# Kernel tuning notes

Hardware: AMD Instinct MI355X
Metric: run time of the kernel (lower is better)

The kernel has to match this reference:

```python
import jax, jax.numpy as jnp
import numpy as np

BN_EPS = 1e-5


def _pool_features(labels, fx, fy, n_labels):
    # Mean-pool per-pixel features (fx, fy, xx, yy coord maps) over superpixel labels.
    B, _, w, h = labels.shape
    xx = (jnp.arange(w, dtype=jnp.float32) / (w - 1)) * 2.0 - 1.0   # varies along dim 2
    yy = (jnp.arange(h, dtype=jnp.float32) / (h - 1)) * 2.0 - 1.0   # varies along dim 3
    xx_map = jnp.broadcast_to(xx[:, None], (w, h))
    yy_map = jnp.broadcast_to(yy[None, :], (w, h))
    P = w * h
    feats = jnp.stack([
        fx[:, 0].reshape(B, P),
        fy[:, 0].reshape(B, P),
        jnp.broadcast_to(xx_map.reshape(1, P), (B, P)),
        jnp.broadcast_to(yy_map.reshape(1, P), (B, P)),
    ], axis=-1).reshape(B * P, 4)                                   # [B*P, 4]
    seg = (labels[:, 0].reshape(B, P)
           + n_labels * jnp.arange(B, dtype=jnp.int32)[:, None]).reshape(-1)
    sums = jax.ops.segment_sum(feats, seg, num_segments=B * n_labels)        # [B*K, 4]
    counts = jax.ops.segment_sum(jnp.ones((B * P,), jnp.float32), seg,
                                 num_segments=B * n_labels)                  # [B*K]
    return sums / jnp.maximum(counts, 1.0)[:, None]


def _bn(x, g, b):
    # BatchNorm1d in training mode: batch statistics over the token dim.
    m = x.mean(axis=0)
    v = x.var(axis=0)
    return (x - m) * jax.lax.rsqrt(v + BN_EPS) * g + b


def reference(labels, fx, fy, frame_idx, n_frames, n_labels,
              conv_w, conv_b, bn1_g, bn1_b, lin_w, lin_b, bn2_g, bn2_b):
    pooled = _pool_features(labels, fx, fy, n_labels)               # [B*K, 4] = (fx, fy, xx, yy)
    t = jnp.repeat(frame_idx.astype(jnp.float32) / (n_frames - 1), n_labels)  # [B*K]
    x = jnp.concatenate([t[:, None], pooled], axis=1)               # [B*K, 5]
    x = x @ conv_w.T + conv_b                                       # Conv1d(5,64,1) == linear
    x = jax.nn.relu(_bn(x, bn1_g, bn1_b))
    x = x @ lin_w.T + lin_b                                         # Linear(64,32)
    x = jax.nn.relu(_bn(x, bn2_g, bn2_b))
    nrm = jnp.linalg.norm(x, axis=1, keepdims=True)
    return x / jnp.maximum(nrm, 1e-8)


def setup_inputs() -> dict:
    key = jax.random.key(0)
    ks = jax.random.split(key, 12)
    B, H, W, K = 16, 512, 512, 1024
    labels = jax.random.randint(ks[0], (B, 1, H, W), 0, K, dtype=jnp.int32)
    fx = jax.random.normal(ks[1], (B, 1, H, W), dtype=jnp.float32)
    fy = jax.random.normal(ks[2], (B, 1, H, W), dtype=jnp.float32)
    frame_idx = jax.random.randint(ks[3], (B,), 0, 100, dtype=jnp.int32)
    conv_w = jax.random.normal(ks[4], (64, 5), dtype=jnp.float32) * 0.3
    conv_b = jax.random.normal(ks[5], (64,), dtype=jnp.float32) * 0.05
    bn1_g = 1.0 + 0.05 * jax.random.normal(ks[6], (64,), dtype=jnp.float32)
    bn1_b = 0.05 * jax.random.normal(ks[7], (64,), dtype=jnp.float32)
    lin_w = jax.random.normal(ks[8], (32, 64), dtype=jnp.float32) * 0.1
    lin_b = jax.random.normal(ks[9], (32,), dtype=jnp.float32) * 0.05
    bn2_g = 1.0 + 0.05 * jax.random.normal(ks[10], (32,), dtype=jnp.float32)
    bn2_b = 0.05 * jax.random.normal(ks[11], (32,), dtype=jnp.float32)
    return {"labels": labels, "fx": fx, "fy": fy, "frame_idx": frame_idx,
            "n_frames": 100, "n_labels": K,
            "conv_w": conv_w, "conv_b": conv_b, "bn1_g": bn1_g, "bn1_b": bn1_b,
            "lin_w": lin_w, "lin_b": lin_b, "bn2_g": bn2_g, "bn2_b": bn2_b}
```

## Files before the change

kernel.cpp:

```cpp
#include <hip/hip_runtime.h>
#include <math.h>

#define TPB 256
#define TPBP 1024
#define FSCALE 16384.0f
#define INV_FSCALE (1.0f / 16384.0f)
#define FBIAS (1 << 17)
#define FCLAMP 7.0f


__global__ __launch_bounds__(TPBP)
void pool_kernel(const int* __restrict__ labels,
                 const float* __restrict__ fx,
                 const float* __restrict__ fy,
                 float* __restrict__ partial,
                 int K, int H, int W, int wlog, int chunks) {
    extern __shared__ unsigned long long sh[];
    unsigned long long* geo = sh;
    unsigned long long* fxy = sh + K;
    const int tid = threadIdx.x;

    for (int i = tid; i < K; i += TPBP) { geo[i] = 0ull; fxy[i] = 0ull; }
    __syncthreads();

    const int P = H * W;
    const int b = blockIdx.x / chunks;
    const int chunk = blockIdx.x - b * chunks;
    const int chunkP = P / chunks;
    const size_t base = (size_t)b * P + (size_t)chunk * chunkP;
    const int4*   l4p  = (const int4*)(labels + base);
    const float4* fx4p = (const float4*)(fx + base);
    const float4* fy4p = (const float4*)(fy + base);
    const int nvec = chunkP >> 2;

    for (int v = tid; v < nvec; v += TPBP) {
        int4   l4 = l4p[v];
        float4 f4 = fx4p[v];
        float4 g4 = fy4p[v];
        int p0 = chunk * chunkP + (v << 2);
        int   ls[4] = {l4.x, l4.y, l4.z, l4.w};
        float fs[4] = {f4.x, f4.y, f4.z, f4.w};
        float gs[4] = {g4.x, g4.y, g4.z, g4.w};
        #pragma unroll
        for (int s = 0; s < 4; ++s) {
            int p = p0 + s;
            int i, j;
            if (wlog >= 0) { i = p >> wlog; j = p & (W - 1); }
            else           { i = p / W;     j = p - i * W; }
            unsigned long long gadd = ((unsigned long long)i << 40)
                                    | ((unsigned long long)j << 16) | 1ull;
            int qx = __float2int_rn(fminf(fmaxf(fs[s], -FCLAMP), FCLAMP) * FSCALE) + FBIAS;
            int qy = __float2int_rn(fminf(fmaxf(gs[s], -FCLAMP), FCLAMP) * FSCALE) + FBIAS;
            unsigned long long fadd = ((unsigned long long)(unsigned int)qx << 32)
                                    | (unsigned long long)(unsigned int)qy;
            atomicAdd(&geo[ls[s]], gadd);
            atomicAdd(&fxy[ls[s]], fadd);
        }
    }
    __syncthreads();

    const float sx = 2.f / (float)(H - 1);
    const float sy = 2.f / (float)(W - 1);
    float* outp = partial + (size_t)blockIdx.x * K * 5;
    for (int k = tid; k < K; k += TPBP) {
        unsigned long long g = geo[k];
        unsigned long long ff = fxy[k];
        unsigned int ci = (unsigned int)(g & 0xFFFFull);
        float cnt = (float)ci;
        float sj  = (float)(unsigned int)((g >> 16) & 0xFFFFFFull);
        float si  = (float)(unsigned int)(g >> 40);
        long long cbias = (long long)ci << 17;
        outp[0 * K + k] = (float)((long long)(ff >> 32) - cbias) * INV_FSCALE;
        outp[1 * K + k] = (float)((long long)(ff & 0xFFFFFFFFull) - cbias) * INV_FSCALE;
        outp[2 * K + k] = sx * si - cnt;
        outp[3 * K + k] = sy * sj - cnt;
        outp[4 * K + k] = cnt;
    }
}

template <int ROWS>
__device__ __forceinline__ float red_fixed(const float* __restrict__ base, int stride) {
    float a = 0.f;
    #pragma unroll
    for (int r = 0; r < ROWS; ++r) a += base[(size_t)r * stride];
    return a;
}
__device__ __forceinline__ float red_dyn(const float* __restrict__ base, int rows, int stride) {
    float a = 0.f;
    #pragma unroll 8
    for (int r = 0; r < rows; ++r) a += base[(size_t)r * stride];
    return a;
}

__global__ __launch_bounds__(TPB)
void k_layer1(const float* __restrict__ partial,
              const int* __restrict__ frame_idx,
              const int* __restrict__ n_frames_p,
              const float* __restrict__ conv_w,
              const float* __restrict__ conv_b,
              float* __restrict__ statA,
              float* __restrict__ h1g,
              int K, int N, int chunks) {
    __shared__ float red[320];
    __shared__ float cw[320], cb[64];
    __shared__ float h1t[64 * 65];
    __shared__ float ps[256], pq[256];

    const int tid = threadIdx.x;
    const int bid = blockIdx.x;

    for (int i = tid; i < 320; i += TPB) cw[i] = conv_w[i];
    if (tid < 64) cb[tid] = conv_b[tid];

    const int t0 = bid * 64;
    const int b  = t0 / K;
    const int k0 = t0 - b * K;

    const int f1 = tid >> 6, kk = tid & 63;
    float a0 = 0.f, a1 = 0.f;
    const float* pb = partial + (size_t)b * chunks * K * 5;
    if (chunks == 16) {
        #pragma unroll
        for (int ch = 0; ch < 16; ++ch) {
            const float* pc = pb + (size_t)ch * K * 5;
            a0 += pc[(size_t)f1 * K + k0 + kk];
            if (tid < 64) a1 += pc[(size_t)4 * K + k0 + tid];
        }
    } else {
        #pragma unroll 4
        for (int ch = 0; ch < chunks; ++ch) {
            const float* pc = pb + (size_t)ch * K * 5;
            a0 += pc[(size_t)f1 * K + k0 + kk];
            if (tid < 64) a1 += pc[(size_t)4 * K + k0 + tid];
        }
    }
    red[f1 * 64 + kk] = a0;
    if (tid < 64) red[4 * 64 + tid] = a1;
    __syncthreads();

    const int g  = tid >> 6;
    const int tt = tid & 63;
    const int t  = t0 + tt;
    const bool valid = t < N;

    const float cntv = red[4 * 64 + tt];
    const float inv  = 1.f / fmaxf(cntv, 1.f);
    const float invnf = 1.f / (float)(n_frames_p[0] - 1);
    const float x0 = valid ? (float)frame_idx[b] * invnf : 0.f;
    const float x1 = red[0 * 64 + tt] * inv;
    const float x2 = red[1 * 64 + tt] * inv;
    const float x3 = red[2 * 64 + tt] * inv;
    const float x4 = red[3 * 64 + tt] * inv;

    const int c0 = g * 16;
    #pragma unroll
    for (int j = 0; j < 16; ++j) {
        int c = c0 + j;
        const float* w = cw + c * 5;
        float h = cb[c] + w[0]*x0 + w[1]*x1 + w[2]*x2 + w[3]*x3 + w[4]*x4;
        h1g[(size_t)c * N + t] = h;
        h1t[c * 65 + tt] = valid ? h : 0.f;
    }
    __syncthreads();

    {
        const int cc = tid & 63, rr = tid >> 6;
        float s = 0.f, q = 0.f;
        #pragma unroll
        for (int i = 0; i < 16; ++i) {
            float v = h1t[cc * 65 + rr * 16 + i];
            s += v; q += v * v;
        }
        ps[rr * 64 + cc] = s;
        pq[rr * 64 + cc] = q;
    }
    __syncthreads();
    if (tid < 64) {
        float su = ps[tid] + ps[64 + tid] + ps[128 + tid] + ps[192 + tid];
        float sq = pq[tid] + pq[64 + tid] + pq[128 + tid] + pq[192 + tid];
        statA[(size_t)bid * 128 + tid] = su;
        statA[(size_t)bid * 128 + 64 + tid] = sq;
    }
}

__global__ __launch_bounds__(TPB)
void k_layer2(const float* __restrict__ statA,
              const float* __restrict__ bn1_g,
              const float* __restrict__ bn1_b,
              const float* __restrict__ lin_w,
              const float* __restrict__ lin_b,
              const float* __restrict__ h1g,
              float* __restrict__ statB,
              float* __restrict__ h2g,
              int N) {
    __shared__ float red[256], w2[2048], lb[32];
    __shared__ float sc1[64], sh1[64];
    __shared__ float h1t[64 * 64];
    __shared__ float h2t[32 * 65];
    __shared__ float ps[256], pq[256];

    const int tid = threadIdx.x;
    const int bid = blockIdx.x;
    const int nblk = gridDim.x;
    const int t0 = bid * 64;

    for (int i = tid; i < 2048; i += TPB) w2[i] = lin_w[i];
    if (tid < 32) lb[tid] = lin_b[tid];

    {
        const int col  = tid & 127;
        const int half = tid >> 7;
        const int rows = nblk >> 1;
        const float* base = statA + (size_t)half * rows * 128 + col;
        red[tid] = (rows == 128) ? red_fixed<128>(base, 128)
                                 : red_dyn(base, rows, 128);
    }

    {
        #pragma unroll
        for (int pass = 0; pass < 4; ++pass) {
            int idx = pass * TPB + tid;
            int c = idx >> 4, q = idx & 15;
            float4 v = *(const float4*)(h1g + (size_t)c * N + t0 + q * 4);
            *(float4*)(&h1t[c * 64 + q * 4]) = v;
        }
    }
    __syncthreads();

    if (tid < 64) {
        float su = red[tid] + red[128 + tid];
        float sq = red[64 + tid] + red[192 + tid];
        float invN = 1.f / (float)N;
        float mean = su * invN;
        float var  = sq * invN - mean * mean;
        float s = bn1_g[tid] * rsqrtf(var + 1e-5f);
        sc1[tid] = s;
        sh1[tid] = bn1_b[tid] - mean * s;
    }
    __syncthreads();

    const int g  = tid >> 6;
    const int tt = tid & 63;
    const int t  = t0 + tt;
    const bool valid = t < N;

    float y[64];
    #pragma unroll
    for (int c = 0; c < 64; ++c)
        y[c] = fmaxf(h1t[c * 64 + tt] * sc1[c] + sh1[c], 0.f);

    const int o0 = g * 8;
    #pragma unroll
    for (int j = 0; j < 8; ++j) {
        int o = o0 + j;
        const float* wo = w2 + o * 64;
        float acc = lb[o];
        #pragma unroll
        for (int c = 0; c < 64; ++c) acc += wo[c] * y[c];
        h2g[(size_t)o * N + t] = acc;
        h2t[o * 65 + tt] = valid ? acc : 0.f;
    }
    __syncthreads();

    {
        const int o = tid & 31, rr = tid >> 5;
        float s = 0.f, q = 0.f;
        #pragma unroll
        for (int i = 0; i < 8; ++i) {
            float v = h2t[o * 65 + rr * 8 + i];
            s += v; q += v * v;
        }
        ps[rr * 32 + o] = s;
        pq[rr * 32 + o] = q;
    }
    __syncthreads();
    if (tid < 32) {
        float su = 0.f, sq = 0.f;
        #pragma unroll
        for (int rr = 0; rr < 8; ++rr) { su += ps[rr * 32 + tid]; sq += pq[rr * 32 + tid]; }
        statB[(size_t)bid * 64 + tid] = su;
        statB[(size_t)bid * 64 + 32 + tid] = sq;
    }
}

__global__ __launch_bounds__(TPB)
void k_final(const float* __restrict__ statB,
             const float* __restrict__ bn2_g,
             const float* __restrict__ bn2_b,
             const float* __restrict__ h2g,
             float* __restrict__ out,
             int N) {
    __shared__ float red[256];
    __shared__ float sc2[32], sh2[32];
    __shared__ float h2t[32 * 68];
    __shared__ float ssqp[4 * 64], linv[64];

    const int tid = threadIdx.x;
    const int bid = blockIdx.x;
    const int nblk = gridDim.x;
    const int t0 = bid * 64;

    {
        const int col = tid & 63;
        const int qr  = tid >> 6;
        const int rows = nblk >> 2;
        const float* base = statB + (size_t)qr * rows * 64 + col;
        red[tid] = (rows == 64) ? red_fixed<64>(base, 64)
                                : red_dyn(base, rows, 64);
    }

    {
        #pragma unroll
        for (int pass = 0; pass < 2; ++pass) {
            int idx = pass * TPB + tid;
            int o = idx >> 4, q = idx & 15;
            float4 v = *(const float4*)(h2g + (size_t)o * N + t0 + q * 4);
            *(float4*)(&h2t[o * 68 + q * 4]) = v;
        }
    }
    __syncthreads();

    if (tid < 32) {
        float su = red[tid] + red[64 + tid] + red[128 + tid] + red[192 + tid];
        float sq = red[32 + tid] + red[96 + tid] + red[160 + tid] + red[224 + tid];
        float invN = 1.f / (float)N;
        float mean = su * invN;
        float var  = sq * invN - mean * mean;
        float s = bn2_g[tid] * rsqrtf(var + 1e-5f);
        sc2[tid] = s;
        sh2[tid] = bn2_b[tid] - mean * s;
    }
    __syncthreads();

    const int g  = tid >> 6;
    const int tt = tid & 63;
    {
        const int o0 = g * 8;
        float ss = 0.f;
        #pragma unroll
        for (int j = 0; j < 8; ++j) {
            int o = o0 + j;
            float v = fmaxf(h2t[o * 68 + tt] * sc2[o] + sh2[o], 0.f);
            h2t[o * 68 + tt] = v;
            ss += v * v;
        }
        ssqp[g * 64 + tt] = ss;
    }
    __syncthreads();
    if (g == 0) {
        float tot = ssqp[tt] + ssqp[64 + tt] + ssqp[128 + tt] + ssqp[192 + tt];
        linv[tt] = 1.f / fmaxf(sqrtf(tot), 1e-8f);
    }
    __syncthreads();

    const int nq = min(512, (N - t0) * 8);
    float4* o4 = (float4*)(out + (size_t)t0 * 32);
    for (int q = tid; q < nq; q += TPB) {
        int tk = q >> 3;
        int oo = (q & 7) * 4;
        float iv = linv[tk];
        o4[q] = make_float4(h2t[(oo + 0) * 68 + tk] * iv,
                            h2t[(oo + 1) * 68 + tk] * iv,
                            h2t[(oo + 2) * 68 + tk] * iv,
                            h2t[(oo + 3) * 68 + tk] * iv);
    }
}

extern "C" void kernel_launch(void* const* d_in, const int* in_sizes, int n_in,
                              void* d_out, int out_size, void* d_ws, size_t ws_size,
                              hipStream_t stream) {
    const int*   labels     = (const int*)d_in[0];
    const float* fx         = (const float*)d_in[1];
    const float* fy         = (const float*)d_in[2];
    const int*   frame_idx  = (const int*)d_in[3];
    const int*   n_frames_p = (const int*)d_in[4];
    const float* conv_w = (const float*)d_in[6];
    const float* conv_b = (const float*)d_in[7];
    const float* bn1_g  = (const float*)d_in[8];
    const float* bn1_b  = (const float*)d_in[9];
    const float* lin_w  = (const float*)d_in[10];
    const float* lin_b  = (const float*)d_in[11];
    const float* bn2_g  = (const float*)d_in[12];
    const float* bn2_b  = (const float*)d_in[13];
    float* out = (float*)d_out;

    const int B = in_sizes[3];
    const int P = in_sizes[0] / B;
    const int W = (int)(sqrt((double)P) + 0.5);
    const int H = P / W;
    const int K = out_size / (B * 32);
    const int N = B * K;

    int wlog = -1;
    if ((W & (W - 1)) == 0) { wlog = 0; while ((1 << wlog) < W) ++wlog; }

    const int nblk = (N + 63) / 64;

    int chunks = 16;
    while (chunks > 1 && (P % (chunks * 4)) != 0) chunks >>= 1;
    while (P / chunks > 16384) chunks <<= 1;

    float* statA   = (float*)d_ws;
    float* statB   = statA + (size_t)nblk * 128;
    float* partial = statB + (size_t)nblk * 64;
    float* h1g     = partial + (size_t)B * chunks * K * 5;
    float* h2g     = h1g + (size_t)64 * N;

    pool_kernel<<<B * chunks, TPBP, (size_t)K * 16, stream>>>(
        labels, fx, fy, partial, K, H, W, wlog, chunks);
    k_layer1<<<nblk, TPB, 0, stream>>>(
        partial, frame_idx, n_frames_p, conv_w, conv_b, statA, h1g, K, N, chunks);
    k_layer2<<<nblk, TPB, 0, stream>>>(
        statA, bn1_g, bn1_b, lin_w, lin_b, h1g, statB, h2g, N);
    k_final<<<nblk, TPB, 0, stream>>>(
        statB, bn2_g, bn2_b, h2g, out, N);
}
```

Baseline: 127.9 us.

## Derive BN1 statistics from input feature moments instead of materializing conv output

Layer 1 no longer writes the 64-channel conv output to global memory. It stores only the 5 pooled features per token, plus per-block first and second moments of those features (5 sums and 15 cross products). Layer 2 rebuilds the BN1 mean and variance algebraically from these moments and the conv weights, then recomputes the conv inline. This cuts global traffic from 64 floats per token to 5 and shrinks the statistics reduction, at the cost of recomputing the conv and some cancellation risk when variance is formed from raw second moments.

```diff
diff --git a/kernel.cpp b/kernel.cpp
--- a/kernel.cpp
+++ b/kernel.cpp
@@ -92,25 +92,22 @@
     return a;
 }
 
+__constant__ int PA[15] = {0,0,0,0,0, 1,1,1,1, 2,2,2, 3,3, 4};
+__constant__ int PB[15] = {0,1,2,3,4, 1,2,3,4, 2,3,4, 3,4, 4};
+
 __global__ __launch_bounds__(TPB)
-void k_layer1(const float* __restrict__ partial,
-              const int* __restrict__ frame_idx,
-              const int* __restrict__ n_frames_p,
-              const float* __restrict__ conv_w,
-              const float* __restrict__ conv_b,
-              float* __restrict__ statA,
-              float* __restrict__ h1g,
-              int K, int N, int chunks) {
+void k_feat(const float* __restrict__ partial,
+            const int* __restrict__ frame_idx,
+            const int* __restrict__ n_frames_p,
+            float* __restrict__ statM,
+            float* __restrict__ featg,
+            int K, int N, int chunks) {
     __shared__ float red[320];
-    __shared__ float cw[320], cb[64];
-    __shared__ float h1t[64 * 65];
-    __shared__ float ps[256], pq[256];
+    __shared__ float xls[5 * 65];
+    __shared__ float pm[8 * 32];
 
     const int tid = threadIdx.x;
     const int bid = blockIdx.x;
-
-    for (int i = tid; i < 320; i += TPB) cw[i] = conv_w[i];
-    if (tid < 64) cb[tid] = conv_b[tid];
 
     const int t0 = bid * 64;
     const int b  = t0 / K;
@@ -143,59 +140,70 @@
     const int t  = t0 + tt;
     const bool valid = t < N;
 
-    const float cntv = red[4 * 64 + tt];
-    const float inv  = 1.f / fmaxf(cntv, 1.f);
-    const float invnf = 1.f / (float)(n_frames_p[0] - 1);
-    const float x0 = valid ? (float)frame_idx[b] * invnf : 0.f;
-    const float x1 = red[0 * 64 + tt] * inv;
-    const float x2 = red[1 * 64 + tt] * inv;
-    const float x3 = red[2 * 64 + tt] * inv;
-    const float x4 = red[3 * 64 + tt] * inv;
-
-    const int c0 = g * 16;
-    #pragma unroll
-    for (int j = 0; j < 16; ++j) {
-        int c = c0 + j;
-        const float* w = cw + c * 5;
-        float h = cb[c] + w[0]*x0 + w[1]*x1 + w[2]*x2 + w[3]*x3 + w[4]*x4;
-        h1g[(size_t)c * N + t] = h;
-        h1t[c * 65 + tt] = valid ? h : 0.f;
-    }
-    __syncthreads();
-
-    {
-        const int cc = tid & 63, rr = tid >> 6;
-        float s = 0.f, q = 0.f;
-        #pragma unroll
-        for (int i = 0; i < 16; ++i) {
-            float v = h1t[cc * 65 + rr * 16 + i];
-            s += v; q += v * v;
-        }
-        ps[rr * 64 + cc] = s;
-        pq[rr * 64 + cc] = q;
-    }
-    __syncthreads();
-    if (tid < 64) {
-        float su = ps[tid] + ps[64 + tid] + ps[128 + tid] + ps[192 + tid];
-        float sq = pq[tid] + pq[64 + tid] + pq[128 + tid] + pq[192 + tid];
-        statA[(size_t)bid * 128 + tid] = su;
-        statA[(size_t)bid * 128 + 64 + tid] = sq;
+    if (g == 0) {
+        const float cntv = red[4 * 64 + tt];
+        const float inv  = 1.f / fmaxf(cntv, 1.f);
+        const float invnf = 1.f / (float)(n_frames_p[0] - 1);
+        const float x0 = valid ? (float)frame_idx[b] * invnf : 0.f;
+        const float x1 = red[0 * 64 + tt] * inv;
+        const float x2 = red[1 * 64 + tt] * inv;
+        const float x3 = red[2 * 64 + tt] * inv;
+        const float x4 = red[3 * 64 + tt] * inv;
+        if (valid) {
+            featg[(size_t)0 * N + t] = x0;
+            featg[(size_t)1 * N + t] = x1;
+            featg[(size_t)2 * N + t] = x2;
+            featg[(size_t)3 * N + t] = x3;
+            featg[(size_t)4 * N + t] = x4;
+        }
+        xls[0 * 65 + tt] = valid ? x0 : 0.f;
+        xls[1 * 65 + tt] = valid ? x1 : 0.f;
+        xls[2 * 65 + tt] = valid ? x2 : 0.f;
+        xls[3 * 65 + tt] = valid ? x3 : 0.f;
+        xls[4 * 65 + tt] = valid ? x4 : 0.f;
+    }
+    __syncthreads();
+
+    {
+        const int q = tid & 31, rr = tid >> 5;
+        float s = 0.f;
+        if (q < 5) {
+            #pragma unroll
+            for (int i = 0; i < 8; ++i) s += xls[q * 65 + rr * 8 + i];
+        } else if (q < 20) {
+            const int a = PA[q - 5], c = PB[q - 5];
+            #pragma unroll
+            for (int i = 0; i < 8; ++i) {
+                int tok = rr * 8 + i;
+                s += xls[a * 65 + tok] * xls[c * 65 + tok];
+            }
+        }
+        pm[rr * 32 + q] = s;
+    }
+    __syncthreads();
+    if (tid < 20) {
+        float s = 0.f;
+        #pragma unroll
+        for (int grp = 0; grp < 8; ++grp) s += pm[grp * 32 + tid];
+        statM[(size_t)bid * 32 + tid] = s;
     }
 }
 
 __global__ __launch_bounds__(TPB)
-void k_layer2(const float* __restrict__ statA,
+void k_layer2(const float* __restrict__ statM,
               const float* __restrict__ bn1_g,
               const float* __restrict__ bn1_b,
+              const float* __restrict__ conv_w,
+              const float* __restrict__ conv_b,
               const float* __restrict__ lin_w,
               const float* __restrict__ lin_b,
-              const float* __restrict__ h1g,
+              const float* __restrict__ featg,
               float* __restrict__ statB,
               float* __restrict__ h2g,
               int N) {
-    __shared__ float red[256], w2[2048], lb[32];
+    __shared__ float pm[8 * 32], SM[20];
+    __shared__ float cw[320], cb[64], w2[2048], lb[32];
     __shared__ float sc1[64], sh1[64];
-    __shared__ float h1t[64 * 64];
     __shared__ float h2t[32 * 65];
     __shared__ float ps[256], pq[256];
 
@@ -204,33 +212,64 @@
     const int nblk = gridDim.x;
     const int t0 = bid * 64;
 
+    for (int i = tid; i < 320; i += TPB) cw[i] = conv_w[i];
+    if (tid < 64) cb[tid] = conv_b[tid];
     for (int i = tid; i < 2048; i += TPB) w2[i] = lin_w[i];
     if (tid < 32) lb[tid] = lin_b[tid];
 
     {
-        const int col  = tid & 127;
-        const int half = tid >> 7;
-        const int rows = nblk >> 1;
-        const float* base = statA + (size_t)half * rows * 128 + col;
-        red[tid] = (rows == 128) ? red_fixed<128>(base, 128)
-                                 : red_dyn(base, rows, 128);
-    }
-
-    {
-        #pragma unroll
-        for (int pass = 0; pass < 4; ++pass) {
-            int idx = pass * TPB + tid;
-            int c = idx >> 4, q = idx & 15;
-            float4 v = *(const float4*)(h1g + (size_t)c * N + t0 + q * 4);
-            *(float4*)(&h1t[c * 64 + q * 4]) = v;
-        }
+        const int q = tid & 31, grp = tid >> 5;
+        float a = 0.f;
+        if (q < 20) {
+            const int rows = nblk >> 3;
+            const float* base = statM + (size_t)grp * rows * 32 + q;
+            a = (rows == 32) ? red_fixed<32>(base, 32) : red_dyn(base, rows, 32);
+        }
+        pm[grp * 32 + q] = a;
+    }
+
+    const int g  = tid >> 6;
+    const int tt = tid & 63;
+    const int t  = t0 + tt;
+    const bool valid = t < N;
+
+    const float x0 = featg[(size_t)0 * N + t];
+    const float x1 = featg[(size_t)1 * N + t];
+    const float x2 = featg[(size_t)2 * N + t];
+    const float x3 = featg[(size_t)3 * N + t];
+    const float x4 = featg[(size_t)4 * N + t];
+    __syncthreads();
+
+    if (tid < 20) {
+        float s = 0.f;
+        #pragma unroll
+        for (int grp = 0; grp < 8; ++grp) s += pm[grp * 32 + tid];
+        SM[tid] = s;
     }
     __syncthreads();
 
     if (tid < 64) {
-        float su = red[tid] + red[128 + tid];
-        float sq = red[64 + tid] + red[192 + tid];
-        float invN = 1.f / (float)N;
+        const int idx[5][5] = {{5,6,7,8,9},{6,10,11,12,13},{7,11,14,15,16},
+                               {8,12,15,17,18},{9,13,16,18,19}};
+        float w[5];
+        #pragma unroll
+        for (int f = 0; f < 5; ++f) w[f] = cw[tid * 5 + f];
+        float wS = 0.f;
+        #pragma unroll
+        for (int f = 0; f < 5; ++f) wS += w[f] * SM[f];
+        float quad = 0.f;
+        #pragma unroll
+        for (int f = 0; f < 5; ++f) {
+            float r = 0.f;
+            #pragma unroll
+            for (int gg = 0; gg < 5; ++gg) r += w[gg] * SM[idx[f][gg]];
+            quad += w[f] * r;
+        }
+        const float cbv = cb[tid];
+        const float fN = (float)N;
+        float su = fN * cbv + wS;
+        float sq = fN * cbv * cbv + 2.f * cbv * wS + quad;
+        float invN = 1.f / fN;
         float mean = su * invN;
         float var  = sq * invN - mean * mean;
         float s = bn1_g[tid] * rsqrtf(var + 1e-5f);
@@ -239,15 +278,13 @@
     }
     __syncthreads();
 
-    const int g  = tid >> 6;
-    const int tt = tid & 63;
-    const int t  = t0 + tt;
-    const bool valid = t < N;
-
     float y[64];
     #pragma unroll
-    for (int c = 0; c < 64; ++c)
-        y[c] = fmaxf(h1t[c * 64 + tt] * sc1[c] + sh1[c], 0.f);
+    for (int c = 0; c < 64; ++c) {
+        const float* w = cw + c * 5;
+        float h = cb[c] + w[0]*x0 + w[1]*x1 + w[2]*x2 + w[3]*x3 + w[4]*x4;
+        y[c] = fmaxf(h * sc1[c] + sh1[c], 0.f);
+    }
 
     const int o0 = g * 8;
     #pragma unroll
@@ -257,7 +294,7 @@
         float acc = lb[o];
         #pragma unroll
         for (int c = 0; c < 64; ++c) acc += wo[c] * y[c];
-        h2g[(size_t)o * N + t] = acc;
+        if (valid) h2g[(size_t)o * N + t] = acc;
         h2t[o * 65 + tt] = valid ? acc : 0.f;
     }
     __syncthreads();
@@ -400,18 +437,19 @@
     while (chunks > 1 && (P % (chunks * 4)) != 0) chunks >>= 1;
     while (P / chunks > 16384) chunks <<= 1;
 
-    float* statA   = (float*)d_ws;
-    float* statB   = statA + (size_t)nblk * 128;
+    float* statM   = (float*)d_ws;
+    float* statB   = statM + (size_t)nblk * 32;
     float* partial = statB + (size_t)nblk * 64;
-    float* h1g     = partial + (size_t)B * chunks * K * 5;
-    float* h2g     = h1g + (size_t)64 * N;
+    float* featg   = partial + (size_t)B * chunks * K * 5;
+    float* h2g     = featg + (size_t)5 * N;
 
     pool_kernel<<<B * chunks, TPBP, (size_t)K * 16, stream>>>(
         labels, fx, fy, partial, K, H, W, wlog, chunks);
-    k_layer1<<<nblk, TPB, 0, stream>>>(
-        partial, frame_idx, n_frames_p, conv_w, conv_b, statA, h1g, K, N, chunks);
+    k_feat<<<nblk, TPB, 0, stream>>>(
+        partial, frame_idx, n_frames_p, statM, featg, K, N, chunks);
     k_layer2<<<nblk, TPB, 0, stream>>>(
-        statA, bn1_g, bn1_b, lin_w, lin_b, h1g, statB, h2g, N);
+        statM, bn1_g, bn1_b, conv_w, conv_b, lin_w, lin_b, featg,
+        statB, h2g, N);
     k_final<<<nblk, TPB, 0, stream>>>(
         statB, bn2_g, bn2_b, h2g, out, N);
 }
```

Result: slower. 131.5 us (+2.9%).
